# Kernel tuning notes

Measured on AMD Instinct MI355X. Metric: run time of the kernel, lower is better.

## Reference

```python
import math
import jax, jax.numpy as jnp
import numpy as np

MODEL_DIM = 4096
NUM_EXPERTS = 64
NUM_TOKENS = 8192
CAPACITY_FACTOR = 1.0


def setup_inputs() -> dict:
    key = jax.random.key(0)
    kx, kw = jax.random.split(key)
    x = jax.random.normal(kx, (NUM_TOKENS, MODEL_DIM), dtype=jnp.float32)
    # nn.Linear weight: [num_experts, model_dim]
    W = jax.random.normal(kw, (NUM_EXPERTS, MODEL_DIM), dtype=jnp.float32) * (1.0 / math.sqrt(MODEL_DIM))
    return {"x": x, "W": W}


def reference(x, W):
    # gating projection (no bias), cast to fp32 as in top1gating
    logits = jnp.matmul(x, W.T).astype(jnp.float32)  # [S, E]
    num_tokens, num_experts = logits.shape
    capacity = int(CAPACITY_FACTOR * math.ceil(num_tokens / num_experts))

    indices1_s = jnp.argmax(logits, axis=1)                        # [S]
    gates = jax.nn.softmax(logits, axis=1)                         # [S, E]
    mask1 = jax.nn.one_hot(indices1_s, num_experts, dtype=jnp.float32)  # [S, E]
    gates1_s = jnp.sum(gates * mask1, axis=1)                      # [S]
    # per-expert running position of each routed token
    locations1 = jnp.cumsum(mask1, axis=0) - 1.0                   # [S, E]
    locations1_s = jnp.sum(locations1 * mask1, axis=1)             # [S]

    return (indices1_s.astype(jnp.int32),
            capacity,
            locations1_s.astype(jnp.int32),
            gates1_s,
            num_experts)
```

## Files before the change

### kernel.cpp

```cpp
#include <hip/hip_runtime.h>
#include <math.h>

#define NTOK 8192
#define MDIM 4096
#define NEXP 64
#define CAPACITY 128.0f

#define OFF_IDX  0
#define OFF_CAP  8192
#define OFF_LOC  8193
#define OFF_GATE 16385
#define OFF_NE   24577

#define NSLICE 4
#define KSLICE (MDIM / NSLICE)
#define KC     64
#define NCHUNK (KSLICE / KC)

#define WS_CNT_OFF  0
#define WS_RK_OFF   8192
#define WS_PART_OFF 16384
#define WS_W_OFF    (WS_PART_OFF + NSLICE * NTOK * NEXP)

using bf16x8 = __attribute__((ext_vector_type(8))) short;
using f32x4  = __attribute__((ext_vector_type(4))) float;

static __device__ __forceinline__ unsigned short f2bf(float f) {
    union { float f; unsigned u; } v; v.f = f;
    unsigned r = v.u + 0x7fffu + ((v.u >> 16) & 1u);
    return (unsigned short)(r >> 16);
}
static __device__ __forceinline__ float bf2f(unsigned short h) {
    union { unsigned u; float f; } v; v.u = ((unsigned)h) << 16;
    return v.f;
}

__global__ __launch_bounds__(256) void prep_w(
    const float* __restrict__ W, unsigned short* __restrict__ Ws)
{
    const int gid = blockIdx.x * 256 + threadIdx.x;
    const int e   = gid >> 10;
    const int f4  = gid & 1023;
    float4 v = ((const float4*)W)[e * 1024 + f4];
    float av[4] = {v.x, v.y, v.z, v.w};
    unsigned short h[3][4];
    #pragma unroll
    for (int j = 0; j < 4; ++j) {
        float a = av[j];
        unsigned short b1 = f2bf(a);  float r1 = a  - bf2f(b1);
        unsigned short b2 = f2bf(r1); float r2 = r1 - bf2f(b2);
        unsigned short b3 = f2bf(r2);
        h[0][j] = b1; h[1][j] = b2; h[2][j] = b3;
    }
    #pragma unroll
    for (int t = 0; t < 3; ++t)
        *(ushort4*)&Ws[((size_t)(t * 64 + e)) * MDIM + f4 * 4] =
            make_ushort4(h[t][0], h[t][1], h[t][2], h[t][3]);
}

__global__ __launch_bounds__(256, 2) void gate_mfma(
    const float* __restrict__ x,
    const unsigned short* __restrict__ Ws,
    float* __restrict__ part)
{
    __shared__ __align__(16) unsigned short xs[2][3][64][72];

    const int tid  = threadIdx.x;
    const int lane = tid & 63;
    const int wv   = tid >> 6;
    const int tok0 = blockIdx.x * 64;
    const int slice = blockIdx.y;
    const int k0   = slice * KSLICE;

    const float4* __restrict__ x4 = (const float4*)x;

    float4 xr[4];

    auto load_regs = [&](int c) {
        #pragma unroll
        for (int q = 0; q < 4; ++q) {
            const int f  = q * 256 + tid;
            const int tr = f >> 4;
            const int k4 = f & 15;
            xr[q] = x4[(size_t)(tok0 + tr) * (MDIM / 4) + (k0 >> 2) + c * 16 + k4];
        }
    };

    auto cvt_write = [&](int b) {
        #pragma unroll
        for (int q = 0; q < 4; ++q) {
            const int f  = q * 256 + tid;
            const int tr = f >> 4;
            const int k4 = f & 15;
            float av[4] = {xr[q].x, xr[q].y, xr[q].z, xr[q].w};
            unsigned short h[3][4];
            #pragma unroll
            for (int j = 0; j < 4; ++j) {
                float a = av[j];
                unsigned short b1 = f2bf(a);  float r1 = a  - bf2f(b1);
                unsigned short b2 = f2bf(r1); float r2 = r1 - bf2f(b2);
                unsigned short b3 = f2bf(r2);
                h[0][j] = b1; h[1][j] = b2; h[2][j] = b3;
            }
            #pragma unroll
            for (int t = 0; t < 3; ++t)
                *(ushort4*)&xs[b][t][tr][k4 * 4] =
                    make_ushort4(h[t][0], h[t][1], h[t][2], h[t][3]);
        }
    };

    f32x4 acc[4];
    #pragma unroll
    for (int nt = 0; nt < 4; ++nt) acc[nt] = (f32x4){0.f, 0.f, 0.f, 0.f};

    auto compute = [&](int b, int c) {
        const int m = lane & 15;
        const int g = lane >> 4;
        #pragma unroll
        for (int ks = 0; ks < 2; ++ks) {
            const int kk = ks * 32 + g * 8;
            bf16x8 a[3];
            #pragma unroll
            for (int t = 0; t < 3; ++t)
                a[t] = *(const bf16x8*)&xs[b][t][wv * 16 + m][kk];
            bf16x8 w[3][4];
            #pragma unroll
            for (int t = 0; t < 3; ++t)
                #pragma unroll
                for (int nt = 0; nt < 4; ++nt)
                    w[t][nt] = *(const bf16x8*)
                        &Ws[((size_t)(t * 64 + nt * 16 + m)) * MDIM + k0 + c * KC + kk];
            #pragma unroll
            for (int nt = 0; nt < 4; ++nt)
                acc[nt] = __builtin_amdgcn_mfma_f32_16x16x32_bf16(a[2], w[0][nt], acc[nt], 0, 0, 0);
            #pragma unroll
            for (int nt = 0; nt < 4; ++nt)
                acc[nt] = __builtin_amdgcn_mfma_f32_16x16x32_bf16(a[0], w[2][nt], acc[nt], 0, 0, 0);
            #pragma unroll
            for (int nt = 0; nt < 4; ++nt)
                acc[nt] = __builtin_amdgcn_mfma_f32_16x16x32_bf16(a[1], w[1][nt], acc[nt], 0, 0, 0);
            #pragma unroll
            for (int nt = 0; nt < 4; ++nt)
                acc[nt] = __builtin_amdgcn_mfma_f32_16x16x32_bf16(a[1], w[0][nt], acc[nt], 0, 0, 0);
            #pragma unroll
            for (int nt = 0; nt < 4; ++nt)
                acc[nt] = __builtin_amdgcn_mfma_f32_16x16x32_bf16(a[0], w[1][nt], acc[nt], 0, 0, 0);
            #pragma unroll
            for (int nt = 0; nt < 4; ++nt)
                acc[nt] = __builtin_amdgcn_mfma_f32_16x16x32_bf16(a[0], w[0][nt], acc[nt], 0, 0, 0);
        }
    };

    load_regs(0);
    cvt_write(0);
    __syncthreads();

    for (int c = 0; c < NCHUNK; ++c) {
        const int cur = c & 1;
        if (c + 1 < NCHUNK) load_regs(c + 1);
        compute(cur, c);
        if (c + 1 < NCHUNK) cvt_write(cur ^ 1);
        __syncthreads();
    }

    #pragma unroll
    for (int nt = 0; nt < 4; ++nt)
        #pragma unroll
        for (int r = 0; r < 4; ++r) {
            const int tokr = tok0 + wv * 16 + (lane >> 4) * 4 + r;
            part[((size_t)slice * NTOK + tokr) * 64 + nt * 16 + (lane & 15)] = acc[nt][r];
        }
}

template<int S>
__global__ __launch_bounds__(256) void reduce_count(
    const float* __restrict__ part,
    float* __restrict__ out,
    int* __restrict__ cnt,
    int* __restrict__ rk)
{
    __shared__ int eidx[64];

    const int tid  = threadIdx.x;
    const int lane = tid & 63;
    const int wv   = tid >> 6;
    const int tok0 = blockIdx.x * 64;
    const int trel = wv * 16 + (lane >> 2);
    const int tok  = tok0 + trel;
    const int q    = lane & 3;

    const float4* __restrict__ p4 = (const float4*)part;

    float4 a[4];
    #pragma unroll
    for (int r = 0; r < 4; ++r) a[r] = make_float4(0.f, 0.f, 0.f, 0.f);
    for (int s = 0; s < S; ++s) {
        #pragma unroll
        for (int r = 0; r < 4; ++r) {
            float4 v = p4[((size_t)s * NTOK + tok) * 16 + q * 4 + r];
            a[r].x += v.x; a[r].y += v.y; a[r].z += v.z; a[r].w += v.w;
        }
    }

    float vals[16];
    #pragma unroll
    for (int r = 0; r < 4; ++r) {
        vals[r * 4 + 0] = a[r].x; vals[r * 4 + 1] = a[r].y;
        vals[r * 4 + 2] = a[r].z; vals[r * 4 + 3] = a[r].w;
    }

    float bm = vals[0];
    int   be = q * 16;
    #pragma unroll
    for (int j = 1; j < 16; ++j)
        if (vals[j] > bm) { bm = vals[j]; be = q * 16 + j; }
    #pragma unroll
    for (int off = 1; off <= 2; off <<= 1) {
        float om = __shfl_xor(bm, off, 64);
        int   oe = __shfl_xor(be, off, 64);
        if (om > bm || (om == bm && oe < be)) { bm = om; be = oe; }
    }

    float es = 0.f;
    #pragma unroll
    for (int j = 0; j < 16; ++j) es += expf(vals[j] - bm);
    #pragma unroll
    for (int off = 1; off <= 2; off <<= 1)
        es += __shfl_xor(es, off, 64);

    if (q == 0) {
        out[OFF_IDX  + tok] = (float)be;
        out[OFF_GATE + tok] = 1.0f / es;
        eidx[trel] = be;
    }
    __syncthreads();

    if (tid < 64) {
        const int e = eidx[tid];
        const unsigned long long lt =
            (tid == 0) ? 0ull : ((~0ull) >> (64 - tid));
        unsigned long long mymask = 0;
        int myrk = 0;
        for (int ee = 0; ee < 64; ++ee) {
            unsigned long long mb = __ballot(e == ee);
            if (tid == ee) mymask = mb;
            if (e == ee)   myrk   = (int)__popcll(mb & lt);
        }
        cnt[blockIdx.x * 64 + tid] = (int)__popcll(mymask);
        rk[tok0 + tid] = myrk;
    }
    if (tid == 0 && blockIdx.x == 0) {
        out[OFF_CAP] = CAPACITY;
        out[OFF_NE]  = (float)NEXP;
    }
}

__global__ __launch_bounds__(1024) void scan_final(
    const float* __restrict__ idxf,
    const int* __restrict__ cnt,
    const int* __restrict__ rk,
    float* __restrict__ out)
{
    __shared__ int lcnt[128 * 64];
    __shared__ int wtot[16 * 64];

    const int tid  = threadIdx.x;
    const int lane = tid & 63;
    const int w    = tid >> 6;

    #pragma unroll
    for (int j = 0; j < 8; ++j) lcnt[j * 1024 + tid] = cnt[j * 1024 + tid];
    __syncthreads();

    {
        int sum = 0;
        #pragma unroll
        for (int j = 0; j < 8; ++j) sum += lcnt[(w * 8 + j) * 64 + lane];
        wtot[w * 64 + lane] = sum;
    }
    __syncthreads();

    if (tid < 64) {
        int run = 0;
        #pragma unroll
        for (int w2 = 0; w2 < 16; ++w2) {
            int t = wtot[w2 * 64 + tid];
            wtot[w2 * 64 + tid] = run;
            run += t;
        }
    }
    __syncthreads();

    {
        int run = wtot[w * 64 + lane];
        #pragma unroll
        for (int j = 0; j < 8; ++j) {
            int c = w * 8 + j;
            int v = lcnt[c * 64 + lane];
            lcnt[c * 64 + lane] = run;
            run += v;
        }
    }
    __syncthreads();

    #pragma unroll
    for (int j = 0; j < 8; ++j) {
        int s = j * 1024 + tid;
        int e = (int)idxf[s];
        out[OFF_LOC + s] = (float)(lcnt[(s >> 6) * 64 + e] + rk[s]);
    }
}

extern "C" void kernel_launch(void* const* d_in, const int* in_sizes, int n_in,
                              void* d_out, int out_size, void* d_ws, size_t ws_size,
                              hipStream_t stream)
{
    const float* x = (const float*)d_in[0];
    const float* W = (const float*)d_in[1];
    float* out = (float*)d_out;

    int*   cnt  = (int*)d_ws + WS_CNT_OFF;
    int*   rk   = (int*)d_ws + WS_RK_OFF;
    float* part = (float*)d_ws + WS_PART_OFF;
    unsigned short* Ws = (unsigned short*)((int*)d_ws + WS_W_OFF);


    prep_w<<<256, 256, 0, stream>>>(W, Ws);
    gate_mfma<<<dim3(128, NSLICE), 256, 0, stream>>>(x, Ws, part);
    reduce_count<NSLICE><<<128, 256, 0, stream>>>(part, out, cnt, rk);
    scan_final<<<1, 1024, 0, stream>>>(out + OFF_IDX, cnt, rk, out);
}
```

Before: 264.8 us.

## Load x directly into MFMA fragment registers, dropping LDS staging and barriers

The gating GEMM kernel no longer stages x through shared memory. Each lane now loads the fp32 values it needs for its MFMA A-fragment straight from global memory, splits them into three bf16 parts in registers, and prefetches two chunks ahead using two register buffers. This removes LDS writes and reads and the per-chunk __syncthreads. In exchange, global x loads are less coalesced (each lane reads 32-byte pieces from different rows) and register pressure is higher.

```diff
diff --git a/kernel.cpp b/kernel.cpp
--- a/kernel.cpp
+++ b/kernel.cpp
@@ -63,112 +63,100 @@
     const unsigned short* __restrict__ Ws,
     float* __restrict__ part)
 {
-    __shared__ __align__(16) unsigned short xs[2][3][64][72];
-
-    const int tid  = threadIdx.x;
-    const int lane = tid & 63;
-    const int wv   = tid >> 6;
-    const int tok0 = blockIdx.x * 64;
+    const int tid   = threadIdx.x;
+    const int lane  = tid & 63;
+    const int wv    = tid >> 6;
+    const int m     = lane & 15;
+    const int g     = lane >> 4;
+    const int tok0  = blockIdx.x * 64;
     const int slice = blockIdx.y;
-    const int k0   = slice * KSLICE;
-
-    const float4* __restrict__ x4 = (const float4*)x;
-
-    float4 xr[4];
-
-    auto load_regs = [&](int c) {
-        #pragma unroll
-        for (int q = 0; q < 4; ++q) {
-            const int f  = q * 256 + tid;
-            const int tr = f >> 4;
-            const int k4 = f & 15;
-            xr[q] = x4[(size_t)(tok0 + tr) * (MDIM / 4) + (k0 >> 2) + c * 16 + k4];
-        }
+    const int k0    = slice * KSLICE;
+    const int tok   = tok0 + wv * 16 + m;
+
+    const float* __restrict__ xp =
+        x + (size_t)tok * MDIM + k0 + g * 8;
+    const unsigned short* __restrict__ wp =
+        Ws + (size_t)m * MDIM + k0 + g * 8;
+
+    f32x4 acc[4];
+    #pragma unroll
+    for (int nt = 0; nt < 4; ++nt) acc[nt] = (f32x4){0.f, 0.f, 0.f, 0.f};
+
+    auto loadx = [&](float4* d, int c) {
+        const float* p = xp + c * KC;
+        d[0] = *(const float4*)(p);
+        d[1] = *(const float4*)(p + 4);
+        d[2] = *(const float4*)(p + 32);
+        d[3] = *(const float4*)(p + 36);
     };
 
-    auto cvt_write = [&](int b) {
-        #pragma unroll
-        for (int q = 0; q < 4; ++q) {
-            const int f  = q * 256 + tid;
-            const int tr = f >> 4;
-            const int k4 = f & 15;
-            float av[4] = {xr[q].x, xr[q].y, xr[q].z, xr[q].w};
-            unsigned short h[3][4];
+    auto cvt = [&](float4 lo, float4 hi, bf16x8& r0, bf16x8& r1, bf16x8& r2) {
+        float f[8] = {lo.x, lo.y, lo.z, lo.w, hi.x, hi.y, hi.z, hi.w};
+        #pragma unroll
+        for (int j = 0; j < 8; ++j) {
+            float a = f[j];
+            unsigned short b1 = f2bf(a);  float t1 = a  - bf2f(b1);
+            unsigned short b2 = f2bf(t1); float t2 = t1 - bf2f(b2);
+            unsigned short b3 = f2bf(t2);
+            r0[j] = (short)b1; r1[j] = (short)b2; r2[j] = (short)b3;
+        }
+    };
+
+    auto step = [&](const bf16x8* a, bf16x8 w[3][4]) {
+        #pragma unroll
+        for (int nt = 0; nt < 4; ++nt)
+            acc[nt] = __builtin_amdgcn_mfma_f32_16x16x32_bf16(a[2], w[0][nt], acc[nt], 0, 0, 0);
+        #pragma unroll
+        for (int nt = 0; nt < 4; ++nt)
+            acc[nt] = __builtin_amdgcn_mfma_f32_16x16x32_bf16(a[0], w[2][nt], acc[nt], 0, 0, 0);
+        #pragma unroll
+        for (int nt = 0; nt < 4; ++nt)
+            acc[nt] = __builtin_amdgcn_mfma_f32_16x16x32_bf16(a[1], w[1][nt], acc[nt], 0, 0, 0);
+        #pragma unroll
+        for (int nt = 0; nt < 4; ++nt)
+            acc[nt] = __builtin_amdgcn_mfma_f32_16x16x32_bf16(a[1], w[0][nt], acc[nt], 0, 0, 0);
+        #pragma unroll
+        for (int nt = 0; nt < 4; ++nt)
+            acc[nt] = __builtin_amdgcn_mfma_f32_16x16x32_bf16(a[0], w[1][nt], acc[nt], 0, 0, 0);
+        #pragma unroll
+        for (int nt = 0; nt < 4; ++nt)
+            acc[nt] = __builtin_amdgcn_mfma_f32_16x16x32_bf16(a[0], w[0][nt], acc[nt], 0, 0, 0);
+    };
+
+    auto body = [&](float4* buf, int c) {
+        bf16x8 w0[3][4], w1[3][4];
+        const unsigned short* q = wp + c * KC;
+        #pragma unroll
+        for (int t = 0; t < 3; ++t)
             #pragma unroll
-            for (int j = 0; j < 4; ++j) {
-                float a = av[j];
-                unsigned short b1 = f2bf(a);  float r1 = a  - bf2f(b1);
-                unsigned short b2 = f2bf(r1); float r2 = r1 - bf2f(b2);
-                unsigned short b3 = f2bf(r2);
-                h[0][j] = b1; h[1][j] = b2; h[2][j] = b3;
+            for (int nt = 0; nt < 4; ++nt) {
+                const unsigned short* r = q + (size_t)(t * 64 + nt * 16) * MDIM;
+                w0[t][nt] = *(const bf16x8*)(r);
+                w1[t][nt] = *(const bf16x8*)(r + 32);
             }
-            #pragma unroll
-            for (int t = 0; t < 3; ++t)
-                *(ushort4*)&xs[b][t][tr][k4 * 4] =
-                    make_ushort4(h[t][0], h[t][1], h[t][2], h[t][3]);
-        }
+        bf16x8 a0[3], a1[3];
+        cvt(buf[0], buf[1], a0[0], a0[1], a0[2]);
+        cvt(buf[2], buf[3], a1[0], a1[1], a1[2]);
+        const int cn = (c + 2 < NCHUNK) ? c + 2 : NCHUNK - 1;
+        loadx(buf, cn);
+        step(a0, w0);
+        step(a1, w1);
     };
 
-    f32x4 acc[4];
-    #pragma unroll
-    for (int nt = 0; nt < 4; ++nt) acc[nt] = (f32x4){0.f, 0.f, 0.f, 0.f};
-
-    auto compute = [&](int b, int c) {
-        const int m = lane & 15;
-        const int g = lane >> 4;
-        #pragma unroll
-        for (int ks = 0; ks < 2; ++ks) {
-            const int kk = ks * 32 + g * 8;
-            bf16x8 a[3];
-            #pragma unroll
-            for (int t = 0; t < 3; ++t)
-                a[t] = *(const bf16x8*)&xs[b][t][wv * 16 + m][kk];
-            bf16x8 w[3][4];
-            #pragma unroll
-            for (int t = 0; t < 3; ++t)
-                #pragma unroll
-                for (int nt = 0; nt < 4; ++nt)
-                    w[t][nt] = *(const bf16x8*)
-                        &Ws[((size_t)(t * 64 + nt * 16 + m)) * MDIM + k0 + c * KC + kk];
-            #pragma unroll
-            for (int nt = 0; nt < 4; ++nt)
-                acc[nt] = __builtin_amdgcn_mfma_f32_16x16x32_bf16(a[2], w[0][nt], acc[nt], 0, 0, 0);
-            #pragma unroll
-            for (int nt = 0; nt < 4; ++nt)
-                acc[nt] = __builtin_amdgcn_mfma_f32_16x16x32_bf16(a[0], w[2][nt], acc[nt], 0, 0, 0);
-            #pragma unroll
-            for (int nt = 0; nt < 4; ++nt)
-                acc[nt] = __builtin_amdgcn_mfma_f32_16x16x32_bf16(a[1], w[1][nt], acc[nt], 0, 0, 0);
-            #pragma unroll
-            for (int nt = 0; nt < 4; ++nt)
-                acc[nt] = __builtin_amdgcn_mfma_f32_16x16x32_bf16(a[1], w[0][nt], acc[nt], 0, 0, 0);
-            #pragma unroll
-            for (int nt = 0; nt < 4; ++nt)
-                acc[nt] = __builtin_amdgcn_mfma_f32_16x16x32_bf16(a[0], w[1][nt], acc[nt], 0, 0, 0);
-            #pragma unroll
-            for (int nt = 0; nt < 4; ++nt)
-                acc[nt] = __builtin_amdgcn_mfma_f32_16x16x32_bf16(a[0], w[0][nt], acc[nt], 0, 0, 0);
-        }
-    };
-
-    load_regs(0);
-    cvt_write(0);
-    __syncthreads();
-
-    for (int c = 0; c < NCHUNK; ++c) {
-        const int cur = c & 1;
-        if (c + 1 < NCHUNK) load_regs(c + 1);
-        compute(cur, c);
-        if (c + 1 < NCHUNK) cvt_write(cur ^ 1);
-        __syncthreads();
+    float4 xa[4], xb[4];
+    loadx(xa, 0);
+    loadx(xb, 1);
+    for (int cc = 0; cc < NCHUNK; cc += 2) {
+        body(xa, cc);
+        body(xb, cc + 1);
     }
 
     #pragma unroll
     for (int nt = 0; nt < 4; ++nt)
         #pragma unroll
         for (int r = 0; r < 4; ++r) {
-            const int tokr = tok0 + wv * 16 + (lane >> 4) * 4 + r;
-            part[((size_t)slice * NTOK + tokr) * 64 + nt * 16 + (lane & 15)] = acc[nt][r];
+            const int tokr = tok0 + wv * 16 + g * 4 + r;
+            part[((size_t)slice * NTOK + tokr) * 64 + nt * 16 + m] = acc[nt][r];
         }
 }
 
@@ -324,7 +312,6 @@
     float* part = (float*)d_ws + WS_PART_OFF;
     unsigned short* Ws = (unsigned short*)((int*)d_ws + WS_W_OFF);
 
-
     prep_w<<<256, 256, 0, stream>>>(W, Ws);
     gate_mfma<<<dim3(128, NSLICE), 256, 0, stream>>>(x, Ws, part);
     reduce_count<NSLICE><<<128, 256, 0, stream>>>(part, out, cnt, rk);
```

Measured after the change: 305.1 us. +15.2%, slower.
